# Kernel tuning notes

Hardware: AMD Instinct MI355X
Metric: run time of the kernel (lower is better)

Reference implementation:

```python
import jax, jax.numpy as jnp
import numpy as np

MARGIN = 0.3


def setup_inputs() -> dict:
    key = jax.random.key(0)
    k1, k2 = jax.random.split(key)
    B, D, N_IDS = 8192, 256, 512
    emb = jax.random.normal(k1, (B, D), dtype=jnp.float32)
    emb = emb / jnp.linalg.norm(emb, axis=1, keepdims=True)  # L2-normalized as docstring states
    labels = jax.random.randint(k2, (B,), 0, N_IDS, dtype=jnp.int64)
    return {"embeddings": emb, "labels": labels}


def reference(embeddings, labels):
    B = embeddings.shape[0]
    # pairwise Euclidean distance via cosine similarity (embeddings are L2-normalized)
    sim = jnp.matmul(embeddings, embeddings.T)              # (B, B)
    dist = jnp.sqrt(jnp.clip(2.0 - 2.0 * sim, 0.0) + 1e-12)
    same = labels[:, None] == labels[None, :]               # (B, B)
    eye = jnp.eye(B, dtype=bool)
    pos_mask = same & ~eye
    neg_mask = ~same
    neg_inf = jnp.asarray(-jnp.inf, dist.dtype)
    pos_inf = jnp.asarray(jnp.inf, dist.dtype)
    dist_ap = jnp.max(jnp.where(pos_mask, dist, neg_inf), axis=1)  # hardest positive per anchor
    dist_an = jnp.min(jnp.where(neg_mask, dist, pos_inf), axis=1)  # hardest negative per anchor
    valid = jnp.any(pos_mask, axis=1) & jnp.any(neg_mask, axis=1)
    # MarginRankingLoss(dist_an, dist_ap, y=1) = mean(relu(dist_ap - dist_an + margin)) over valid anchors
    per = jnp.maximum(dist_ap - dist_an + MARGIN, 0.0)
    per = jnp.where(valid, per, 0.0)
    n_valid = jnp.sum(valid.astype(dist.dtype))
    loss = jnp.where(n_valid > 0, jnp.sum(per) / jnp.maximum(n_valid, 1.0), 0.0)
    return loss
```

## Files before the change

### kernel.cpp

```cpp
#include <hip/hip_runtime.h>
#include <hip/hip_bf16.h>


#define BDIM 8192
#define DDIM 256

typedef short bf16x8 __attribute__((ext_vector_type(8)));
typedef float f32x4  __attribute__((ext_vector_type(4)));
typedef unsigned short u16;

static __device__ __forceinline__ bf16x8 ld_frag(const u16* p) {
    return *reinterpret_cast<const bf16x8*>(p);
}

static __device__ __forceinline__ u16 f2bf(float f) {
    union { float f; unsigned int u; } x; x.f = f;
    unsigned int u = x.u;
    unsigned int r = u + 0x7fffu + ((u >> 16) & 1u);
    return (u16)(r >> 16);
}

static __device__ __forceinline__ void gload_lds16(const u16* g, u16* l) {
    __builtin_amdgcn_global_load_lds(
        (const __attribute__((address_space(1))) unsigned int*)g,
        (__attribute__((address_space(3))) unsigned int*)l, 16, 0, 0);
}

__global__ __launch_bounds__(256) void cvt_init_kernel(const float* __restrict__ in,
                                                       u16* __restrict__ out,
                                                       int* __restrict__ minpos,
                                                       int* __restrict__ maxneg) {
    int i = blockIdx.x * 256 + threadIdx.x;
    const float4 v = reinterpret_cast<const float4*>(in)[i];
    ushort4 o;
    o.x = f2bf(v.x); o.y = f2bf(v.y); o.z = f2bf(v.z); o.w = f2bf(v.w);
    reinterpret_cast<ushort4*>(out)[i] = o;
    if (i < BDIM) {
        minpos[i] = 0x7f800000;
        maxneg[i] = 0;
    }
}

__global__ __launch_bounds__(256, 2) void triplet_main(const u16* __restrict__ Ebf,
                                                       const int* __restrict__ labels,
                                                       int* __restrict__ minpos,
                                                       int* __restrict__ maxneg) {
    __shared__ __align__(16) u16 smem[3][32 * DDIM];
    __shared__ int slab[512];

    const int tid  = threadIdx.x;
    const int w    = tid >> 6;
    const int l    = tid & 63;
    const int quad = l >> 4;
    const int r16  = l & 15;

    const int mblk  = blockIdx.x * 256 + w * 64;
    const int nbase = blockIdx.y * 512;

    slab[tid]       = labels[nbase + tid];
    slab[256 + tid] = labels[nbase + 256 + tid];

    bf16x8 a[4][8];
#pragma unroll
    for (int ms = 0; ms < 4; ++ms) {
        const u16* ap = Ebf + (size_t)(mblk + ms * 16 + r16) * DDIM + quad * 8;
#pragma unroll
        for (int k = 0; k < 8; ++k) a[ms][k] = ld_frag(ap + k * 32);
    }

    int lab_row[4][4];
#pragma unroll
    for (int ms = 0; ms < 4; ++ms)
#pragma unroll
        for (int r = 0; r < 4; ++r)
            lab_row[ms][r] = labels[mblk + ms * 16 + quad * 4 + r];

    float minp[4][4], maxn[4][4];
#pragma unroll
    for (int ms = 0; ms < 4; ++ms)
#pragma unroll
        for (int r = 0; r < 4; ++r) { minp[ms][r] = __builtin_inff(); maxn[ms][r] = -__builtin_inff(); }

    const int qs = quad ^ (r16 & 3);
    const int s4 = (r16 >> 2) & 1;

    auto stage = [&](int t, int buf) {
        const int n1 = nbase + t * 32;
#pragma unroll
        for (int it = 0; it < 4; ++it) {
            const int q = it * 256 + tid;
            const int r = q >> 5;
            const int c = (q & 31) ^ (r & 7);
            gload_lds16(Ebf + ((size_t)(n1 + r) << 8) + c * 8,
                        &smem[buf][0] + it * 2048 + w * 512);
        }
    };

    stage(0, 0);
    stage(1, 1);

    int cur = 0;
#pragma unroll 1
    for (int nn = 0; nn < 16; ++nn) {
        if (nn < 15) asm volatile("s_waitcnt vmcnt(4) lgkmcnt(0)" ::: "memory");
        else         asm volatile("s_waitcnt vmcnt(0) lgkmcnt(0)" ::: "memory");
        __builtin_amdgcn_s_barrier();
        __builtin_amdgcn_sched_barrier(0);

        if (nn + 2 < 16) {
            const int stg = (cur >= 1) ? cur - 1 : 2;
            stage(nn + 2, stg);
        }

        const int n0 = nbase + nn * 32;
        int lab_c[2];
        lab_c[0] = slab[nn * 32 + r16];
        lab_c[1] = slab[nn * 32 + 16 + r16];

        f32x4 acc[4][2];
#pragma unroll
        for (int ms = 0; ms < 4; ++ms)
#pragma unroll
            for (int nt = 0; nt < 2; ++nt)
                acc[ms][nt] = (f32x4){0.f, 0.f, 0.f, 0.f};

        const u16* bb = &smem[cur][0];
        const u16* bnt[2];
#pragma unroll
        for (int nt = 0; nt < 2; ++nt)
            bnt[nt] = bb + (nt * 16 + r16) * DDIM + qs * 8;

        __builtin_amdgcn_s_setprio(1);
#pragma unroll
        for (int k = 0; k < 8; ++k) {
            const int koff = ((k ^ s4) << 5);
            bf16x8 b[2];
#pragma unroll
            for (int nt = 0; nt < 2; ++nt) b[nt] = ld_frag(bnt[nt] + koff);
#pragma unroll
            for (int ms = 0; ms < 4; ++ms)
#pragma unroll
                for (int nt = 0; nt < 2; ++nt)
                    acc[ms][nt] = __builtin_amdgcn_mfma_f32_16x16x32_bf16(
                        a[ms][k], b[nt], acc[ms][nt], 0, 0, 0);
        }
        __builtin_amdgcn_s_setprio(0);

        const bool diagTile = (n0 < mblk + 64) && (mblk < n0 + 32);
        if (__builtin_expect(diagTile, 0)) {
#pragma unroll
            for (int nt = 0; nt < 2; ++nt) {
                const int colg = n0 + nt * 16 + r16;
#pragma unroll
                for (int ms = 0; ms < 4; ++ms)
#pragma unroll
                    for (int r = 0; r < 4; ++r) {
                        const int rowg = mblk + ms * 16 + quad * 4 + r;
                        const float s = acc[ms][nt][r];
                        const bool same = (lab_c[nt] == lab_row[ms][r]);
                        const bool pos  = same && (colg != rowg);
                        minp[ms][r] = fminf(minp[ms][r], pos  ?  s : __builtin_inff());
                        maxn[ms][r] = fmaxf(maxn[ms][r], same ? -__builtin_inff() : s);
                    }
            }
        } else {
#pragma unroll
            for (int nt = 0; nt < 2; ++nt)
#pragma unroll
                for (int ms = 0; ms < 4; ++ms)
#pragma unroll
                    for (int r = 0; r < 4; ++r) {
                        const float s = acc[ms][nt][r];
                        const bool same = (lab_c[nt] == lab_row[ms][r]);
                        minp[ms][r] = fminf(minp[ms][r], same ?  s : __builtin_inff());
                        maxn[ms][r] = fmaxf(maxn[ms][r], same ? -__builtin_inff() : s);
                    }
        }

        cur = (cur == 2) ? 0 : cur + 1;
    }

#pragma unroll
    for (int mask = 1; mask <= 8; mask <<= 1) {
#pragma unroll
        for (int ms = 0; ms < 4; ++ms)
#pragma unroll
            for (int r = 0; r < 4; ++r) {
                minp[ms][r] = fminf(minp[ms][r], __shfl_xor(minp[ms][r], mask, 64));
                maxn[ms][r] = fmaxf(maxn[ms][r], __shfl_xor(maxn[ms][r], mask, 64));
            }
    }
    if (r16 == 0) {
#pragma unroll
        for (int ms = 0; ms < 4; ++ms)
#pragma unroll
            for (int r = 0; r < 4; ++r) {
                const int rowg = mblk + ms * 16 + quad * 4 + r;
                atomicMin(minpos + rowg, __float_as_int(minp[ms][r] + 2.0f));
                atomicMax(maxneg + rowg, __float_as_int(maxn[ms][r] + 2.0f));
            }
    }
}

__global__ __launch_bounds__(1024) void finalize_kernel(const int* __restrict__ minpos,
                                                        const int* __restrict__ maxneg,
                                                        float* __restrict__ out) {
    __shared__ float ssum[16], scnt[16];
    float sum = 0.f, cnt = 0.f;
#pragma unroll
    for (int it = 0; it < 8; ++it) {
        const int i = it * 1024 + threadIdx.x;
        const float mp = __int_as_float(minpos[i]);
        const float mn = __int_as_float(maxneg[i]);
        if (mp < 1e30f && mn > 0.5f) {
            const float dap = sqrtf(fmaxf(6.0f - 2.0f * mp, 0.0f) + 1e-12f);
            const float dan = sqrtf(fmaxf(6.0f - 2.0f * mn, 0.0f) + 1e-12f);
            sum += fmaxf(dap - dan + 0.3f, 0.0f);
            cnt += 1.0f;
        }
    }
#pragma unroll
    for (int off = 32; off > 0; off >>= 1) {
        sum += __shfl_down(sum, off, 64);
        cnt += __shfl_down(cnt, off, 64);
    }
    const int wid = threadIdx.x >> 6;
    if ((threadIdx.x & 63) == 0) { ssum[wid] = sum; scnt[wid] = cnt; }
    __syncthreads();
    if (threadIdx.x == 0) {
        float S = 0.f, C = 0.f;
#pragma unroll
        for (int i = 0; i < 16; ++i) { S += ssum[i]; C += scnt[i]; }
        out[0] = (C > 0.f) ? (S / C) : 0.f;
    }
}

extern "C" void kernel_launch(void* const* d_in, const int* in_sizes, int n_in,
                              void* d_out, int out_size, void* d_ws, size_t ws_size,
                              hipStream_t stream) {
    const float* emb    = (const float*)d_in[0];
    const int*   labels = (const int*)d_in[1];
    float*       out    = (float*)d_out;

    u16* Ebf    = (u16*)d_ws;
    int* minpos = (int*)((char*)d_ws + (size_t)BDIM * DDIM * 2);
    int* maxneg = minpos + BDIM;

    cvt_init_kernel<<<dim3((BDIM * DDIM / 4) / 256), dim3(256), 0, stream>>>(emb, Ebf, minpos, maxneg);
    triplet_main<<<dim3(BDIM / 256, BDIM / 512), dim3(256), 0, stream>>>(Ebf, labels, minpos, maxneg);
    finalize_kernel<<<dim3(1), dim3(1024), 0, stream>>>(minpos, maxneg, out);
}
```

Measured before the change: 107.1 us.

## Exploit symmetry of similarity matrix by computing only upper-triangular tiles

```diff
diff --git a/kernel.cpp b/kernel.cpp
--- a/kernel.cpp
+++ b/kernel.cpp
@@ -46,7 +46,8 @@
                                                        int* __restrict__ minpos,
                                                        int* __restrict__ maxneg) {
     __shared__ __align__(16) u16 smem[3][32 * DDIM];
-    __shared__ int slab[512];
+    __shared__ int slab[256];
+    __shared__ int colmin[256], colmax[256];
 
     const int tid  = threadIdx.x;
     const int w    = tid >> 6;
@@ -54,11 +55,16 @@
     const int quad = l >> 4;
     const int r16  = l & 15;
 
-    const int mblk  = blockIdx.x * 256 + w * 64;
-    const int nbase = blockIdx.y * 512;
-
-    slab[tid]       = labels[nbase + tid];
-    slab[256 + tid] = labels[nbase + 256 + tid];
+    int t = blockIdx.x, bi = 0;
+    while (t >= 32 - bi) { t -= 32 - bi; ++bi; }
+    const int bu = bi + t;
+
+    const int mblk  = bi * 256 + w * 64;
+    const int nbase = bu * 256;
+
+    slab[tid]   = labels[nbase + tid];
+    colmin[tid] = 0x7f800000;
+    colmax[tid] = 0;
 
     bf16x8 a[4][8];
 #pragma unroll
@@ -84,8 +90,8 @@
     const int qs = quad ^ (r16 & 3);
     const int s4 = (r16 >> 2) & 1;
 
-    auto stage = [&](int t, int buf) {
-        const int n1 = nbase + t * 32;
+    auto stage = [&](int tt, int buf) {
+        const int n1 = nbase + tt * 32;
 #pragma unroll
         for (int it = 0; it < 4; ++it) {
             const int q = it * 256 + tid;
@@ -101,80 +107,112 @@
 
     int cur = 0;
 #pragma unroll 1
-    for (int nn = 0; nn < 16; ++nn) {
-        if (nn < 15) asm volatile("s_waitcnt vmcnt(4) lgkmcnt(0)" ::: "memory");
-        else         asm volatile("s_waitcnt vmcnt(0) lgkmcnt(0)" ::: "memory");
+    for (int nn = 0; nn < 8; ++nn) {
+        if (nn < 7) asm volatile("s_waitcnt vmcnt(4) lgkmcnt(0)" ::: "memory");
+        else        asm volatile("s_waitcnt vmcnt(0) lgkmcnt(0)" ::: "memory");
         __builtin_amdgcn_s_barrier();
         __builtin_amdgcn_sched_barrier(0);
 
-        if (nn + 2 < 16) {
+        if (nn + 2 < 8) {
             const int stg = (cur >= 1) ? cur - 1 : 2;
             stage(nn + 2, stg);
         }
 
         const int n0 = nbase + nn * 32;
-        int lab_c[2];
-        lab_c[0] = slab[nn * 32 + r16];
-        lab_c[1] = slab[nn * 32 + 16 + r16];
-
-        f32x4 acc[4][2];
-#pragma unroll
-        for (int ms = 0; ms < 4; ++ms)
+
+        if (n0 + 32 > mblk) {
+            int lab_c[2];
+            lab_c[0] = slab[nn * 32 + r16];
+            lab_c[1] = slab[nn * 32 + 16 + r16];
+
+            f32x4 acc[4][2];
+#pragma unroll
+            for (int ms = 0; ms < 4; ++ms)
+#pragma unroll
+                for (int nt = 0; nt < 2; ++nt)
+                    acc[ms][nt] = (f32x4){0.f, 0.f, 0.f, 0.f};
+
+            const u16* bb = &smem[cur][0];
+            const u16* bnt[2];
 #pragma unroll
             for (int nt = 0; nt < 2; ++nt)
-                acc[ms][nt] = (f32x4){0.f, 0.f, 0.f, 0.f};
-
-        const u16* bb = &smem[cur][0];
-        const u16* bnt[2];
-#pragma unroll
-        for (int nt = 0; nt < 2; ++nt)
-            bnt[nt] = bb + (nt * 16 + r16) * DDIM + qs * 8;
-
-        __builtin_amdgcn_s_setprio(1);
-#pragma unroll
-        for (int k = 0; k < 8; ++k) {
-            const int koff = ((k ^ s4) << 5);
-            bf16x8 b[2];
-#pragma unroll
-            for (int nt = 0; nt < 2; ++nt) b[nt] = ld_frag(bnt[nt] + koff);
-#pragma unroll
-            for (int ms = 0; ms < 4; ++ms)
+                bnt[nt] = bb + (nt * 16 + r16) * DDIM + qs * 8;
+
+            __builtin_amdgcn_s_setprio(1);
+#pragma unroll
+            for (int k = 0; k < 8; ++k) {
+                const int koff = ((k ^ s4) << 5);
+                bf16x8 b[2];
+#pragma unroll
+                for (int nt = 0; nt < 2; ++nt) b[nt] = ld_frag(bnt[nt] + koff);
+#pragma unroll
+                for (int ms = 0; ms < 4; ++ms)
+#pragma unroll
+                    for (int nt = 0; nt < 2; ++nt)
+                        acc[ms][nt] = __builtin_amdgcn_mfma_f32_16x16x32_bf16(
+                            a[ms][k], b[nt], acc[ms][nt], 0, 0, 0);
+            }
+            __builtin_amdgcn_s_setprio(0);
+
+            float cmin[2], cmax[2];
+#pragma unroll
+            for (int nt = 0; nt < 2; ++nt) { cmin[nt] = __builtin_inff(); cmax[nt] = -__builtin_inff(); }
+
+            const bool diagTile = (n0 < mblk + 64) && (mblk < n0 + 32);
+            if (__builtin_expect(diagTile, 0)) {
+#pragma unroll
+                for (int nt = 0; nt < 2; ++nt) {
+                    const int colg = n0 + nt * 16 + r16;
+#pragma unroll
+                    for (int ms = 0; ms < 4; ++ms)
+#pragma unroll
+                        for (int r = 0; r < 4; ++r) {
+                            const int rowg = mblk + ms * 16 + quad * 4 + r;
+                            const float s = acc[ms][nt][r];
+                            const bool same = (lab_c[nt] == lab_row[ms][r]);
+                            const bool pos  = same && (colg != rowg);
+                            const float pv = pos  ?  s : __builtin_inff();
+                            const float nv = same ? -__builtin_inff() : s;
+                            minp[ms][r] = fminf(minp[ms][r], pv);
+                            maxn[ms][r] = fmaxf(maxn[ms][r], nv);
+                            cmin[nt] = fminf(cmin[nt], pv);
+                            cmax[nt] = fmaxf(cmax[nt], nv);
+                        }
+                }
+            } else {
 #pragma unroll
                 for (int nt = 0; nt < 2; ++nt)
-                    acc[ms][nt] = __builtin_amdgcn_mfma_f32_16x16x32_bf16(
-                        a[ms][k], b[nt], acc[ms][nt], 0, 0, 0);
-        }
-        __builtin_amdgcn_s_setprio(0);
-
-        const bool diagTile = (n0 < mblk + 64) && (mblk < n0 + 32);
-        if (__builtin_expect(diagTile, 0)) {
-#pragma unroll
-            for (int nt = 0; nt < 2; ++nt) {
-                const int colg = n0 + nt * 16 + r16;
-#pragma unroll
-                for (int ms = 0; ms < 4; ++ms)
-#pragma unroll
-                    for (int r = 0; r < 4; ++r) {
-                        const int rowg = mblk + ms * 16 + quad * 4 + r;
-                        const float s = acc[ms][nt][r];
-                        const bool same = (lab_c[nt] == lab_row[ms][r]);
-                        const bool pos  = same && (colg != rowg);
-                        minp[ms][r] = fminf(minp[ms][r], pos  ?  s : __builtin_inff());
-                        maxn[ms][r] = fmaxf(maxn[ms][r], same ? -__builtin_inff() : s);
-                    }
-            }
-        } else {
-#pragma unroll
-            for (int nt = 0; nt < 2; ++nt)
-#pragma unroll
-                for (int ms = 0; ms < 4; ++ms)
-#pragma unroll
-                    for (int r = 0; r < 4; ++r) {
-                        const float s = acc[ms][nt][r];
-                        const bool same = (lab_c[nt] == lab_row[ms][r]);
-                        minp[ms][r] = fminf(minp[ms][r], same ?  s : __builtin_inff());
-                        maxn[ms][r] = fmaxf(maxn[ms][r], same ? -__builtin_inff() : s);
-                    }
+#pragma unroll
+                    for (int ms = 0; ms < 4; ++ms)
+#pragma unroll
+                        for (int r = 0; r < 4; ++r) {
+                            const float s = acc[ms][nt][r];
+                            const bool same = (lab_c[nt] == lab_row[ms][r]);
+                            const float pv = same ?  s : __builtin_inff();
+                            const float nv = same ? -__builtin_inff() : s;
+                            minp[ms][r] = fminf(minp[ms][r], pv);
+                            maxn[ms][r] = fmaxf(maxn[ms][r], nv);
+                            cmin[nt] = fminf(cmin[nt], pv);
+                            cmax[nt] = fmaxf(cmax[nt], nv);
+                        }
+            }
+
+#pragma unroll
+            for (int mask = 16; mask <= 32; mask <<= 1) {
+#pragma unroll
+                for (int nt = 0; nt < 2; ++nt) {
+                    cmin[nt] = fminf(cmin[nt], __shfl_xor(cmin[nt], mask, 64));
+                    cmax[nt] = fmaxf(cmax[nt], __shfl_xor(cmax[nt], mask, 64));
+                }
+            }
+            if (quad == 0) {
+#pragma unroll
+                for (int nt = 0; nt < 2; ++nt) {
+                    const int cl = nn * 32 + nt * 16 + r16;
+                    atomicMin(&colmin[cl], __float_as_int(cmin[nt] + 2.0f));
+                    atomicMax(&colmax[cl], __float_as_int(cmax[nt] + 2.0f));
+                }
+            }
         }
 
         cur = (cur == 2) ? 0 : cur + 1;
@@ -200,6 +238,10 @@
                 atomicMax(maxneg + rowg, __float_as_int(maxn[ms][r] + 2.0f));
             }
     }
+
+    __syncthreads();
+    atomicMin(minpos + nbase + tid, colmin[tid]);
+    atomicMax(maxneg + nbase + tid, colmax[tid]);
 }
 
 __global__ __launch_bounds__(1024) void finalize_kernel(const int* __restrict__ minpos,
@@ -247,6 +289,6 @@
     int* maxneg = minpos + BDIM;
 
     cvt_init_kernel<<<dim3((BDIM * DDIM / 4) / 256), dim3(256), 0, stream>>>(emb, Ebf, minpos, maxneg);
-    triplet_main<<<dim3(BDIM / 256, BDIM / 512), dim3(256), 0, stream>>>(Ebf, labels, minpos, maxneg);
+    triplet_main<<<dim3(528), dim3(256), 0, stream>>>(Ebf, labels, minpos, maxneg);
     finalize_kernel<<<dim3(1), dim3(1024), 0, stream>>>(minpos, maxneg, out);
 }
```

After: 113.7 us. 6.1% more time.

## Switch to 64-column tiles with double buffering instead of 32-column triple buffering

Applied to the files above, without the earlier changes.

```diff
diff --git a/kernel.cpp b/kernel.cpp
--- a/kernel.cpp
+++ b/kernel.cpp
@@ -45,7 +45,7 @@
                                                        const int* __restrict__ labels,
                                                        int* __restrict__ minpos,
                                                        int* __restrict__ maxneg) {
-    __shared__ __align__(16) u16 smem[3][32 * DDIM];
+    __shared__ __align__(16) u16 smem[2][64 * DDIM];
     __shared__ int slab[512];
 
     const int tid  = threadIdx.x;
@@ -85,9 +85,9 @@
     const int s4 = (r16 >> 2) & 1;
 
     auto stage = [&](int t, int buf) {
-        const int n1 = nbase + t * 32;
-#pragma unroll
-        for (int it = 0; it < 4; ++it) {
+        const int n1 = nbase + t * 64;
+#pragma unroll
+        for (int it = 0; it < 8; ++it) {
             const int q = it * 256 + tid;
             const int r = q >> 5;
             const int c = (q & 31) ^ (r & 7);
@@ -97,59 +97,50 @@
     };
 
     stage(0, 0);
-    stage(1, 1);
-
-    int cur = 0;
+
 #pragma unroll 1
-    for (int nn = 0; nn < 16; ++nn) {
-        if (nn < 15) asm volatile("s_waitcnt vmcnt(4) lgkmcnt(0)" ::: "memory");
-        else         asm volatile("s_waitcnt vmcnt(0) lgkmcnt(0)" ::: "memory");
+    for (int t = 0; t < 8; ++t) {
+        const int cur = t & 1;
+        const int n0  = nbase + t * 64;
+
+        asm volatile("s_waitcnt vmcnt(0) lgkmcnt(0)" ::: "memory");
         __builtin_amdgcn_s_barrier();
         __builtin_amdgcn_sched_barrier(0);
 
-        if (nn + 2 < 16) {
-            const int stg = (cur >= 1) ? cur - 1 : 2;
-            stage(nn + 2, stg);
-        }
-
-        const int n0 = nbase + nn * 32;
-        int lab_c[2];
-        lab_c[0] = slab[nn * 32 + r16];
-        lab_c[1] = slab[nn * 32 + 16 + r16];
-
-        f32x4 acc[4][2];
+        if (t + 1 < 8) stage(t + 1, cur ^ 1);
+
+        int lab_c[4];
+#pragma unroll
+        for (int nt = 0; nt < 4; ++nt) lab_c[nt] = slab[t * 64 + nt * 16 + r16];
+
+        f32x4 acc[4][4];
 #pragma unroll
         for (int ms = 0; ms < 4; ++ms)
 #pragma unroll
-            for (int nt = 0; nt < 2; ++nt)
+            for (int nt = 0; nt < 4; ++nt)
                 acc[ms][nt] = (f32x4){0.f, 0.f, 0.f, 0.f};
 
         const u16* bb = &smem[cur][0];
-        const u16* bnt[2];
-#pragma unroll
-        for (int nt = 0; nt < 2; ++nt)
-            bnt[nt] = bb + (nt * 16 + r16) * DDIM + qs * 8;
 
         __builtin_amdgcn_s_setprio(1);
 #pragma unroll
-        for (int k = 0; k < 8; ++k) {
-            const int koff = ((k ^ s4) << 5);
-            bf16x8 b[2];
-#pragma unroll
-            for (int nt = 0; nt < 2; ++nt) b[nt] = ld_frag(bnt[nt] + koff);
-#pragma unroll
-            for (int ms = 0; ms < 4; ++ms)
-#pragma unroll
-                for (int nt = 0; nt < 2; ++nt)
+        for (int nt = 0; nt < 4; ++nt) {
+            const u16* bp = bb + (nt * 16 + r16) * DDIM + qs * 8;
+#pragma unroll
+            for (int k = 0; k < 8; ++k) {
+                const bf16x8 b = ld_frag(bp + ((k ^ s4) << 5));
+#pragma unroll
+                for (int ms = 0; ms < 4; ++ms)
                     acc[ms][nt] = __builtin_amdgcn_mfma_f32_16x16x32_bf16(
-                        a[ms][k], b[nt], acc[ms][nt], 0, 0, 0);
+                        a[ms][k], b, acc[ms][nt], 0, 0, 0);
+            }
         }
         __builtin_amdgcn_s_setprio(0);
 
-        const bool diagTile = (n0 < mblk + 64) && (mblk < n0 + 32);
+        const bool diagTile = (n0 < mblk + 64) && (mblk < n0 + 64);
         if (__builtin_expect(diagTile, 0)) {
 #pragma unroll
-            for (int nt = 0; nt < 2; ++nt) {
+            for (int nt = 0; nt < 4; ++nt) {
                 const int colg = n0 + nt * 16 + r16;
 #pragma unroll
                 for (int ms = 0; ms < 4; ++ms)
@@ -165,7 +156,7 @@
             }
         } else {
 #pragma unroll
-            for (int nt = 0; nt < 2; ++nt)
+            for (int nt = 0; nt < 4; ++nt)
 #pragma unroll
                 for (int ms = 0; ms < 4; ++ms)
 #pragma unroll
@@ -176,8 +167,6 @@
                         maxn[ms][r] = fmaxf(maxn[ms][r], same ? -__builtin_inff() : s);
                     }
         }
-
-        cur = (cur == 2) ? 0 : cur + 1;
     }
 
 #pragma unroll
```

Result: slower. 121.4 us (+13.3%).

## Load B fragments directly from global memory instead of LDS staging

Applied to the files above, without the earlier changes.

```diff
diff --git a/kernel.cpp b/kernel.cpp
--- a/kernel.cpp
+++ b/kernel.cpp
@@ -18,12 +18,6 @@
     unsigned int u = x.u;
     unsigned int r = u + 0x7fffu + ((u >> 16) & 1u);
     return (u16)(r >> 16);
-}
-
-static __device__ __forceinline__ void gload_lds16(const u16* g, u16* l) {
-    __builtin_amdgcn_global_load_lds(
-        (const __attribute__((address_space(1))) unsigned int*)g,
-        (__attribute__((address_space(3))) unsigned int*)l, 16, 0, 0);
 }
 
 __global__ __launch_bounds__(256) void cvt_init_kernel(const float* __restrict__ in,
@@ -45,9 +39,6 @@
                                                        const int* __restrict__ labels,
                                                        int* __restrict__ minpos,
                                                        int* __restrict__ maxneg) {
-    __shared__ __align__(16) u16 smem[3][32 * DDIM];
-    __shared__ int slab[512];
-
     const int tid  = threadIdx.x;
     const int w    = tid >> 6;
     const int l    = tid & 63;
@@ -57,9 +48,6 @@
     const int mblk  = blockIdx.x * 256 + w * 64;
     const int nbase = blockIdx.y * 512;
 
-    slab[tid]       = labels[nbase + tid];
-    slab[256 + tid] = labels[nbase + 256 + tid];
-
     bf16x8 a[4][8];
 #pragma unroll
     for (int ms = 0; ms < 4; ++ms) {
@@ -81,41 +69,20 @@
 #pragma unroll
         for (int r = 0; r < 4; ++r) { minp[ms][r] = __builtin_inff(); maxn[ms][r] = -__builtin_inff(); }
 
-    const int qs = quad ^ (r16 & 3);
-    const int s4 = (r16 >> 2) & 1;
-
-    auto stage = [&](int t, int buf) {
-        const int n1 = nbase + t * 32;
-#pragma unroll
-        for (int it = 0; it < 4; ++it) {
-            const int q = it * 256 + tid;
-            const int r = q >> 5;
-            const int c = (q & 31) ^ (r & 7);
-            gload_lds16(Ebf + ((size_t)(n1 + r) << 8) + c * 8,
-                        &smem[buf][0] + it * 2048 + w * 512);
-        }
-    };
-
-    stage(0, 0);
-    stage(1, 1);
-
-    int cur = 0;
+    const u16* bp0 = Ebf + (size_t)(nbase + r16) * DDIM + quad * 8;
+    const u16* bp1 = bp0 + 16 * DDIM;
+
+    bf16x8 b0[2];
+    b0[0] = ld_frag(bp0);
+    b0[1] = ld_frag(bp1);
+
 #pragma unroll 1
     for (int nn = 0; nn < 16; ++nn) {
-        if (nn < 15) asm volatile("s_waitcnt vmcnt(4) lgkmcnt(0)" ::: "memory");
-        else         asm volatile("s_waitcnt vmcnt(0) lgkmcnt(0)" ::: "memory");
-        __builtin_amdgcn_s_barrier();
-        __builtin_amdgcn_sched_barrier(0);
-
-        if (nn + 2 < 16) {
-            const int stg = (cur >= 1) ? cur - 1 : 2;
-            stage(nn + 2, stg);
-        }
-
         const int n0 = nbase + nn * 32;
+
         int lab_c[2];
-        lab_c[0] = slab[nn * 32 + r16];
-        lab_c[1] = slab[nn * 32 + 16 + r16];
+        lab_c[0] = labels[n0 + r16];
+        lab_c[1] = labels[n0 + 16 + r16];
 
         f32x4 acc[4][2];
 #pragma unroll
@@ -124,27 +91,28 @@
             for (int nt = 0; nt < 2; ++nt)
                 acc[ms][nt] = (f32x4){0.f, 0.f, 0.f, 0.f};
 
-        const u16* bb = &smem[cur][0];
-        const u16* bnt[2];
-#pragma unroll
-        for (int nt = 0; nt < 2; ++nt)
-            bnt[nt] = bb + (nt * 16 + r16) * DDIM + qs * 8;
+        const int nstep = (nn < 15) ? 32 * DDIM : 0;
 
         __builtin_amdgcn_s_setprio(1);
 #pragma unroll
         for (int k = 0; k < 8; ++k) {
-            const int koff = ((k ^ s4) << 5);
-            bf16x8 b[2];
-#pragma unroll
-            for (int nt = 0; nt < 2; ++nt) b[nt] = ld_frag(bnt[nt] + koff);
+            bf16x8 b1[2];
+            const int off = (k < 7) ? (k + 1) * 32 : nstep;
+            b1[0] = ld_frag(bp0 + off);
+            b1[1] = ld_frag(bp1 + off);
 #pragma unroll
             for (int ms = 0; ms < 4; ++ms)
 #pragma unroll
                 for (int nt = 0; nt < 2; ++nt)
                     acc[ms][nt] = __builtin_amdgcn_mfma_f32_16x16x32_bf16(
-                        a[ms][k], b[nt], acc[ms][nt], 0, 0, 0);
+                        a[ms][k], b0[nt], acc[ms][nt], 0, 0, 0);
+            b0[0] = b1[0];
+            b0[1] = b1[1];
         }
         __builtin_amdgcn_s_setprio(0);
+
+        bp0 += nstep;
+        bp1 += nstep;
 
         const bool diagTile = (n0 < mblk + 64) && (mblk < n0 + 32);
         if (__builtin_expect(diagTile, 0)) {
@@ -176,8 +144,6 @@
                         maxn[ms][r] = fmaxf(maxn[ms][r], same ? -__builtin_inff() : s);
                     }
         }
-
-        cur = (cur == 2) ? 0 : cur + 1;
     }
 
 #pragma unroll
```

Result: slower. 134.5 us (+25.5%).
